# Performance work log

Hardware: AMD Instinct MI355X
Metric: run time of the kernel (lower is better)

The kernel has to match this reference:

```python
import jax, jax.numpy as jnp
import numpy as np

V, NJ, NCOMP, NBETA = 778, 16, 24, 10
F_CLOSED, N_ANCHOR = 1554, 32
B, NOBJ = 8, 16384
# MANO kinematic tree parents (wrist + 5 fingers x 3 joints)
PARENTS = np.array([-1, 0, 1, 2, 0, 4, 5, 0, 7, 8, 0, 10, 11, 0, 13, 14])


def setup_inputs() -> dict:
    key = jax.random.key(0)
    ks = jax.random.split(key, 12)
    hand_pose = jax.random.normal(ks[0], (B, 3 + 3 + NCOMP), jnp.float32) * 0.1
    obj_points = jax.random.normal(ks[1], (B, NOBJ, 3), jnp.float32) * 0.1
    hand_beta = jax.random.normal(ks[2], (B, NBETA), jnp.float32) * 0.5
    v_template = jax.random.normal(ks[3], (V, 3), jnp.float32) * 0.05
    shapedirs = jax.random.normal(ks[4], (V, 3, NBETA), jnp.float32) * 0.01
    posedirs = jax.random.normal(ks[5], (V, 3, (NJ - 1) * 9), jnp.float32) * 0.01
    J_regressor = jax.nn.softmax(jax.random.normal(ks[6], (NJ, V), jnp.float32), axis=-1)
    lbs_weights = jax.nn.softmax(jax.random.normal(ks[7], (V, NJ), jnp.float32) * 2.0, axis=-1)
    pca_comps = jax.random.normal(ks[8], (NCOMP, (NJ - 1) * 3), jnp.float32) * 0.1
    anchor_weights = jax.nn.softmax(jax.random.normal(ks[9], (N_ANCHOR, 3), jnp.float32), axis=-1)
    closed_faces = jax.random.randint(ks[10], (F_CLOSED, 3), 0, V, jnp.int32)
    anchor_face_idx = jax.random.randint(ks[11], (N_ANCHOR, 3), 0, V, jnp.int32)
    return dict(hand_pose=hand_pose, obj_points=obj_points, hand_beta=hand_beta,
                v_template=v_template, shapedirs=shapedirs, posedirs=posedirs,
                J_regressor=J_regressor, lbs_weights=lbs_weights, pca_comps=pca_comps,
                anchor_weights=anchor_weights, closed_faces=closed_faces,
                anchor_face_idx=anchor_face_idx)


def rodrigues(r):
    # r: [..., 3] axis-angle -> [..., 3, 3] rotation matrix
    theta = jnp.sqrt(jnp.sum(r * r, axis=-1, keepdims=True) + 1e-16)
    k = r / theta
    c = jnp.cos(theta)[..., None]
    s = jnp.sin(theta)[..., None]
    kx, ky, kz = k[..., 0], k[..., 1], k[..., 2]
    zero = jnp.zeros_like(kx)
    K = jnp.stack([zero, -kz, ky, kz, zero, -kx, -ky, kx, zero], axis=-1)
    K = K.reshape(r.shape[:-1] + (3, 3))
    I = jnp.eye(3, dtype=r.dtype)
    return c * I + s * K + (1.0 - c) * k[..., :, None] * k[..., None, :]


def mano_verts(hand_pose, hand_beta, v_template, shapedirs, posedirs,
               J_regressor, lbs_weights, pca_comps):
    b = hand_pose.shape[0]
    trans = hand_pose[:, :3]
    root = hand_pose[:, 3:6]
    hand45 = hand_pose[:, 6:] @ pca_comps  # PCA -> 45-dim pose (flat_hand_mean: no mean add)
    full = jnp.concatenate([root, hand45], axis=-1).reshape(b, NJ, 3)
    R = rodrigues(full)  # [B,16,3,3]
    v_shaped = v_template + jnp.einsum('vdk,bk->bvd', shapedirs, hand_beta)
    J = jnp.einsum('jv,bvd->bjd', J_regressor, v_shaped)  # [B,16,3]
    pose_feat = (R[:, 1:] - jnp.eye(3, dtype=R.dtype)).reshape(b, (NJ - 1) * 9)
    v_posed = v_shaped + jnp.einsum('vdp,bp->bvd', posedirs, pose_feat)

    def make44(Rj, tj):  # [B,3,3],[B,3] -> [B,4,4]
        T = jnp.zeros((b, 4, 4), R.dtype)
        return T.at[:, :3, :3].set(Rj).at[:, :3, 3].set(tj).at[:, 3, 3].set(1.0)

    Ts = [make44(R[:, 0], J[:, 0])]
    for j in range(1, NJ):  # fixed small kinematic chain
        p = int(PARENTS[j])
        Ts.append(jnp.einsum('bmn,bnk->bmk', Ts[p], make44(R[:, j], J[:, j] - J[:, p])))
    T = jnp.stack(Ts, axis=1)  # [B,16,4,4] global joint transforms
    corr = jnp.einsum('bjmn,bjn->bjm', T[..., :3, :3], J)
    A = T.at[..., :3, 3].add(-corr)  # relative-to-rest transforms
    Tw = jnp.einsum('vj,bjmn->bvmn', lbs_weights, A)  # per-vertex skinning transform
    verts = jnp.einsum('bvmn,bvn->bvm', Tw[..., :3, :3], v_posed) + Tw[..., :3, 3]
    return verts + trans[:, None, :]


def vertex_normals(verts, faces):  # verts [B,V,3], faces [F,3]
    def one(v):
        p0, p1, p2 = v[faces[:, 0]], v[faces[:, 1]], v[faces[:, 2]]
        fn = jnp.cross(p1 - p0, p2 - p0)
        vn = (jnp.zeros_like(v).at[faces[:, 0]].add(fn)
              .at[faces[:, 1]].add(fn).at[faces[:, 2]].add(fn))
        return vn / (jnp.linalg.norm(vn, axis=-1, keepdims=True) + 1e-8)
    return jax.vmap(one)(verts)


def reference(hand_pose, obj_points, hand_beta, v_template, shapedirs, posedirs,
              J_regressor, lbs_weights, pca_comps, anchor_weights,
              closed_faces, anchor_face_idx):
    verts = mano_verts(hand_pose, hand_beta, v_template, shapedirs, posedirs,
                       J_regressor, lbs_weights, pca_comps)  # [B,778,3]
    # get_NN: squared cdist obj->hand + argmin (the memory-bound bottleneck)
    d2 = (jnp.sum(obj_points * obj_points, -1, keepdims=True)
          + jnp.sum(verts * verts, -1)[:, None, :]
          - 2.0 * jnp.einsum('bnd,bvd->bnv', obj_points, verts))  # [B,NOBJ,778]
    nn_idx = jnp.argmin(d2, axis=-1)  # [B,NOBJ]
    nn_dist = jnp.take_along_axis(d2, nn_idx[..., None], axis=-1)[..., 0]
    # contact_map_of_m_to_n
    cmap = 1.0 - 2.0 * (jax.nn.sigmoid(100.0 * nn_dist) - 0.5)
    # inter_penetr_loss: interior obj points (behind nearest hand vertex normal)
    normals = vertex_normals(verts, closed_faces)
    nn_vert = jnp.take_along_axis(verts, nn_idx[..., None], axis=1)
    nn_norm = jnp.take_along_axis(normals, nn_idx[..., None], axis=1)
    interior = jnp.sum((nn_vert - obj_points) * nn_norm, axis=-1) > 0.0
    penetration = jnp.sum(jnp.where(interior, nn_dist, 0.0)) / hand_pose.shape[0]
    # AnchorLayer: barycentric anchor points on the hand surface
    contact_candidates = jnp.einsum('ak,bakd->bad', anchor_weights, verts[:, anchor_face_idx])
    return cmap, penetration, verts, contact_candidates
```

## Files before the change

kernel.cpp:

```cpp
#include <hip/hip_runtime.h>
#include <math.h>

#define NV 778
#define NJ 16
#define NCOMP 24
#define NBETA 10
#define FC 1554
#define NA 32
#define NB 8
#define NOBJ 16384
#define VD (NV*3)
#define NSLOT 13

__global__ __launch_bounds__(256) void k_blend(
    const float* __restrict__ hp, const float* __restrict__ pca,
    const float* __restrict__ beta, const float* __restrict__ vt,
    const float* __restrict__ sd, const float* __restrict__ pd,
    float* __restrict__ VS, float* __restrict__ VP, float* __restrict__ pen)
{
    int b = blockIdx.x >> 2, chunk = blockIdx.x & 3, t = threadIdx.x;
    __shared__ float h45[45];
    __shared__ float sR[NJ*9];
    __shared__ float PF[135];
    if (t < 45) {
        float acc = 0.0f;
        for (int k = 0; k < NCOMP; ++k) acc += hp[b*30 + 6 + k] * pca[k*45 + t];
        h45[t] = acc;
    }
    __syncthreads();
    if (t < NJ) {
        float rx, ry, rz;
        if (t == 0) { rx = hp[b*30+3]; ry = hp[b*30+4]; rz = hp[b*30+5]; }
        else        { rx = h45[(t-1)*3]; ry = h45[(t-1)*3+1]; rz = h45[(t-1)*3+2]; }
        float th = sqrtf(rx*rx + ry*ry + rz*rz + 1e-16f);
        float kx = rx/th, ky = ry/th, kz = rz/th;
        float c = cosf(th), s = sinf(th), o = 1.0f - c;
        sR[t*9+0] = c + o*kx*kx;      sR[t*9+1] = -s*kz + o*kx*ky;  sR[t*9+2] =  s*ky + o*kx*kz;
        sR[t*9+3] =  s*kz + o*ky*kx;  sR[t*9+4] = c + o*ky*ky;      sR[t*9+5] = -s*kx + o*ky*kz;
        sR[t*9+6] = -s*ky + o*kz*kx;  sR[t*9+7] =  s*kx + o*kz*ky;  sR[t*9+8] = c + o*kz*kz;
    }
    __syncthreads();
    if (t < 135) {
        int mn = t % 9;
        float d = (mn == 0 || mn == 4 || mn == 8) ? 1.0f : 0.0f;
        PF[t] = sR[9 + t] - d;
    }
    __syncthreads();
    int v = chunk * 195 + t;
    if (t < 195 && v < NV) {
        const float* bb = beta + b * NBETA;
        int i = b * NV + v;
        #pragma unroll
        for (int d = 0; d < 3; ++d) {
            int r = v*3 + d;
            float vs = vt[r];
            const float* s = sd + r * NBETA;
            #pragma unroll
            for (int k = 0; k < NBETA; ++k) vs += s[k] * bb[k];
            float vp = vs;
            const float* p = pd + r * 135;
            for (int k = 0; k < 135; ++k) vp += p[k] * PF[k];
            VS[i*3 + d] = vs;
            VP[i*3 + d] = vp;
        }
    }
    if (blockIdx.x == 0 && t == 0) *pen = 0.0f;
}

__global__ __launch_bounds__(256) void k_skel(
    const float* __restrict__ hp, const float* __restrict__ pca,
    const float* __restrict__ Jreg, const float* __restrict__ VS,
    const float* __restrict__ VP, const float* __restrict__ W,
    const int* __restrict__ faces, const float* __restrict__ aw,
    const int* __restrict__ afi,
    float* __restrict__ verts, float4* __restrict__ PK,
    float* __restrict__ NRM, float* __restrict__ contact)
{
    int b = blockIdx.x, t = threadIdx.x;
    int lane = t & 63, wid = t >> 6;
    __shared__ float h45[45];
    __shared__ float sR[NJ*9];
    __shared__ float sJ[NJ*3];
    __shared__ float sA[NJ*12];
    __shared__ float sv[VD];
    __shared__ float sn[VD];

    if (t < 45) {
        float acc = 0.0f;
        for (int k = 0; k < NCOMP; ++k) acc += hp[b*30 + 6 + k] * pca[k*45 + t];
        h45[t] = acc;
    }
    for (int i = t; i < VD; i += 256) sn[i] = 0.0f;
    __syncthreads();
    if (t < NJ) {
        float rx, ry, rz;
        if (t == 0) { rx = hp[b*30+3]; ry = hp[b*30+4]; rz = hp[b*30+5]; }
        else        { rx = h45[(t-1)*3]; ry = h45[(t-1)*3+1]; rz = h45[(t-1)*3+2]; }
        float th = sqrtf(rx*rx + ry*ry + rz*rz + 1e-16f);
        float kx = rx/th, ky = ry/th, kz = rz/th;
        float c = cosf(th), s = sinf(th), o = 1.0f - c;
        sR[t*9+0] = c + o*kx*kx;      sR[t*9+1] = -s*kz + o*kx*ky;  sR[t*9+2] =  s*ky + o*kx*kz;
        sR[t*9+3] =  s*kz + o*ky*kx;  sR[t*9+4] = c + o*ky*ky;      sR[t*9+5] = -s*kx + o*ky*kz;
        sR[t*9+6] = -s*ky + o*kz*kx;  sR[t*9+7] =  s*kx + o*kz*ky;  sR[t*9+8] = c + o*kz*kz;
    }

    float ac[12];
    #pragma unroll
    for (int q = 0; q < 12; ++q) ac[q] = 0.0f;
    for (int v = lane; v < NV; v += 64) {
        const float* p = VS + (b*NV + v)*3;
        float x = p[0], y = p[1], z = p[2];
        #pragma unroll
        for (int jj = 0; jj < 4; ++jj) {
            float w = Jreg[(4*wid + jj)*NV + v];
            ac[jj*3+0] += w*x; ac[jj*3+1] += w*y; ac[jj*3+2] += w*z;
        }
    }
    #pragma unroll
    for (int q = 0; q < 12; ++q)
        for (int off = 32; off; off >>= 1) ac[q] += __shfl_down(ac[q], off, 64);
    if (lane == 0) {
        #pragma unroll
        for (int q = 0; q < 12; ++q) sJ[(4*wid + q/3)*3 + (q%3)] = ac[q];
    }
    __syncthreads();

    if (t < 3) {
        const int par[NJ] = {-1,0,1,2,0,4,5,0,7,8,0,10,11,0,13,14};
        int m = t;
        float Tr[NJ][3], Tt[NJ];
        Tr[0][0] = sR[m*3+0]; Tr[0][1] = sR[m*3+1]; Tr[0][2] = sR[m*3+2];
        Tt[0] = sJ[m];
        #pragma unroll
        for (int j = 1; j < NJ; ++j) {
            int p = par[j];
            float t0 = sJ[j*3+0] - sJ[p*3+0];
            float t1 = sJ[j*3+1] - sJ[p*3+1];
            float t2 = sJ[j*3+2] - sJ[p*3+2];
            float a0 = Tr[p][0], a1 = Tr[p][1], a2 = Tr[p][2];
            #pragma unroll
            for (int n = 0; n < 3; ++n)
                Tr[j][n] = a0*sR[j*9+n] + a1*sR[j*9+3+n] + a2*sR[j*9+6+n];
            Tt[j] = a0*t0 + a1*t1 + a2*t2 + Tt[p];
        }
        #pragma unroll
        for (int j = 0; j < NJ; ++j) {
            float corr = Tr[j][0]*sJ[j*3] + Tr[j][1]*sJ[j*3+1] + Tr[j][2]*sJ[j*3+2];
            sA[j*12 + m*4 + 0] = Tr[j][0];
            sA[j*12 + m*4 + 1] = Tr[j][1];
            sA[j*12 + m*4 + 2] = Tr[j][2];
            sA[j*12 + m*4 + 3] = Tt[j] - corr;
        }
    }
    __syncthreads();

    float tx = hp[b*30+0], ty = hp[b*30+1], tz = hp[b*30+2];
    for (int v = t; v < NV; v += 256) {
        float acc[12];
        #pragma unroll
        for (int q = 0; q < 12; ++q) acc[q] = 0.0f;
        const float* w = W + v * NJ;
        for (int j = 0; j < NJ; ++j) {
            float wj = w[j];
            #pragma unroll
            for (int q = 0; q < 12; ++q) acc[q] += wj * sA[j*12 + q];
        }
        int i = b*NV + v;
        float px = VP[i*3], py = VP[i*3+1], pz = VP[i*3+2];
        float x = acc[0]*px + acc[1]*py + acc[2]*pz  + acc[3]  + tx;
        float y = acc[4]*px + acc[5]*py + acc[6]*pz  + acc[7]  + ty;
        float z = acc[8]*px + acc[9]*py + acc[10]*pz + acc[11] + tz;
        sv[v*3] = x; sv[v*3+1] = y; sv[v*3+2] = z;
        verts[i*3] = x; verts[i*3+1] = y; verts[i*3+2] = z;
        PK[i] = make_float4(x, y, z, 0.5f*(x*x + y*y + z*z));
    }
    __syncthreads();

    for (int f = t; f < FC; f += 256) {
        int i0 = faces[f*3], i1 = faces[f*3+1], i2 = faces[f*3+2];
        float ax = sv[i1*3+0]-sv[i0*3+0], ay = sv[i1*3+1]-sv[i0*3+1], az = sv[i1*3+2]-sv[i0*3+2];
        float bx = sv[i2*3+0]-sv[i0*3+0], by = sv[i2*3+1]-sv[i0*3+1], bz = sv[i2*3+2]-sv[i0*3+2];
        float cx = ay*bz - az*by, cy = az*bx - ax*bz, cz = ax*by - ay*bx;
        atomicAdd(&sn[i0*3+0], cx); atomicAdd(&sn[i0*3+1], cy); atomicAdd(&sn[i0*3+2], cz);
        atomicAdd(&sn[i1*3+0], cx); atomicAdd(&sn[i1*3+1], cy); atomicAdd(&sn[i1*3+2], cz);
        atomicAdd(&sn[i2*3+0], cx); atomicAdd(&sn[i2*3+1], cy); atomicAdd(&sn[i2*3+2], cz);
    }
    __syncthreads();

    for (int i = t; i < VD; i += 256) NRM[b*VD + i] = sn[i];
    if (t < NA*3) {
        int a = t / 3, d = t % 3;
        float acc = 0.0f;
        #pragma unroll
        for (int k = 0; k < 3; ++k)
            acc += aw[a*3 + k] * sv[afi[a*3 + k]*3 + d];
        contact[b*NA*3 + t] = acc;
    }
}

__global__ __launch_bounds__(256) void k_nn(const float* __restrict__ obj,
                                            const float4* __restrict__ PK,
                                            const float* __restrict__ NRM,
                                            float* __restrict__ cmap,
                                            float* __restrict__ pen)
{
    int b = blockIdx.x >> 6;
    int n = (blockIdx.x & 63) * 256 + threadIdx.x;
    int t = threadIdx.x, lane = t & 63;
    int base = b * NV;

    float4 q[NSLOT];
    #pragma unroll
    for (int j = 0; j < NSLOT; ++j) {
        int idx = j*64 + lane;
        q[j] = (idx < NV) ? PK[base + idx] : make_float4(0.f, 0.f, 0.f, 1e30f);
    }
    const float* o = obj + (b*NOBJ + n)*3;
    float ox = o[0], oy = o[1], oz = o[2];

    float myS = 0.0f;
    int myI = 0;
    for (int p = 0; p < 64; ++p) {
        float bx = __uint_as_float(__builtin_amdgcn_readlane(__float_as_uint(ox), p));
        float by = __uint_as_float(__builtin_amdgcn_readlane(__float_as_uint(oy), p));
        float bz = __uint_as_float(__builtin_amdgcn_readlane(__float_as_uint(oz), p));
        float sb = 1e30f; int jb = 0;
        #pragma unroll
        for (int j = 0; j < NSLOT; ++j) {
            float s = fmaf(-bx, q[j].x, q[j].w);
            s = fmaf(-by, q[j].y, s);
            s = fmaf(-bz, q[j].z, s);
            if (s < sb) { sb = s; jb = j; }
        }
        int ifull = jb*64 + lane;
        float smin = sb;
        #pragma unroll
        for (int m = 1; m < 64; m <<= 1)
            smin = fminf(smin, __shfl_xor(smin, m, 64));
        unsigned long long mk = __ballot(sb == smin);
        int w = __ffsll(mk) - 1;
        int widx = __builtin_amdgcn_readlane(ifull, w);
        if (lane == p) { myS = smin; myI = widx; }
    }

    float osq = ox*ox + oy*oy + oz*oz;
    float d2 = 2.0f * myS + osq;
    cmap[b*NOBJ + n] = 2.0f / (1.0f + expf(100.0f * d2));

    float4 qq = PK[base + myI];
    float nx = NRM[(base + myI)*3 + 0];
    float ny = NRM[(base + myI)*3 + 1];
    float nz = NRM[(base + myI)*3 + 2];
    float dotp = (qq.x - ox)*nx + (qq.y - oy)*ny + (qq.z - oz)*nz;
    float p = (dotp > 0.0f) ? d2 : 0.0f;
    for (int off = 32; off; off >>= 1) p += __shfl_down(p, off, 64);
    __shared__ float wsum[4];
    if (lane == 0) wsum[t >> 6] = p;
    __syncthreads();
    if (t == 0) atomicAdd(pen, (wsum[0] + wsum[1] + wsum[2] + wsum[3]) * (1.0f / NB));
}

extern "C" void kernel_launch(void* const* d_in, const int* in_sizes, int n_in,
                              void* d_out, int out_size, void* d_ws, size_t ws_size,
                              hipStream_t stream)
{
    const float* hp    = (const float*)d_in[0];
    const float* obj   = (const float*)d_in[1];
    const float* beta  = (const float*)d_in[2];
    const float* vt    = (const float*)d_in[3];
    const float* sd    = (const float*)d_in[4];
    const float* pd    = (const float*)d_in[5];
    const float* Jreg  = (const float*)d_in[6];
    const float* W     = (const float*)d_in[7];
    const float* pca   = (const float*)d_in[8];
    const float* aw    = (const float*)d_in[9];
    const int*   faces = (const int*)d_in[10];
    const int*   afi   = (const int*)d_in[11];

    float* out     = (float*)d_out;
    float* cmap    = out;
    float* pen     = out + NB*NOBJ;
    float* verts   = out + NB*NOBJ + 1;
    float* contact = out + NB*NOBJ + 1 + NB*NV*3;

    float* ws  = (float*)d_ws;
    float4* PK = (float4*)ws;
    float* VS  = ws + NB*NV*4;
    float* VP  = VS + NB*NV*3;
    float* NRM = VP + NB*NV*3;

    k_blend<<<NB*4, 256, 0, stream>>>(hp, pca, beta, vt, sd, pd, VS, VP, pen);
    k_skel <<<NB, 256, 0, stream>>>(hp, pca, Jreg, VS, VP, W, faces, aw, afi,
                                    verts, PK, NRM, contact);
    k_nn   <<<NB*64, 256, 0, stream>>>(obj, PK, NRM, cmap, pen);
}
```

Baseline: 166.3 us.

## Fuse blend-shape and skeleton kernels into one per-batch prep kernel

Merges k_blend and k_skel into a single k_prep kernel with one block per batch element. Shaped vertices stay in shared memory and the pose blend is computed inline, which removes the VS/VP global round trip and one kernel launch. It also packs PF and the skinning matrices as float4 in shared memory. The cost is parallelism: the posedirs matvec now runs on 8 blocks instead of 32, so each thread handles more vertices (778 per block of 256).

```diff
diff --git a/kernel.cpp b/kernel.cpp
--- a/kernel.cpp
+++ b/kernel.cpp
@@ -12,22 +12,36 @@
 #define VD (NV*3)
 #define NSLOT 13
 
-__global__ __launch_bounds__(256) void k_blend(
+__global__ __launch_bounds__(256) void k_prep(
     const float* __restrict__ hp, const float* __restrict__ pca,
     const float* __restrict__ beta, const float* __restrict__ vt,
     const float* __restrict__ sd, const float* __restrict__ pd,
-    float* __restrict__ VS, float* __restrict__ VP, float* __restrict__ pen)
+    const float* __restrict__ Jreg, const float* __restrict__ W,
+    const int* __restrict__ faces, const float* __restrict__ aw,
+    const int* __restrict__ afi,
+    float* __restrict__ verts, float4* __restrict__ PK,
+    float* __restrict__ NRM, float* __restrict__ contact,
+    float* __restrict__ pen)
 {
-    int b = blockIdx.x >> 2, chunk = blockIdx.x & 3, t = threadIdx.x;
-    __shared__ float h45[45];
-    __shared__ float sR[NJ*9];
-    __shared__ float PF[135];
+    int b = blockIdx.x, t = threadIdx.x;
+    int lane = t & 63, wid = t >> 6;
+    __shared__ float  h45[45];
+    __shared__ float  sR[NJ*9];
+    __shared__ float4 PF4[34];
+    __shared__ float  sJ[NJ*3];
+    __shared__ float4 sA4[NJ*3];
+    __shared__ float  svs[VD];
+    __shared__ float  sv[VD];
+    __shared__ float  sn[VD];
+
     if (t < 45) {
         float acc = 0.0f;
         for (int k = 0; k < NCOMP; ++k) acc += hp[b*30 + 6 + k] * pca[k*45 + t];
         h45[t] = acc;
     }
-    __syncthreads();
+    for (int i = t; i < VD; i += 256) sn[i] = 0.0f;
+    __syncthreads();
+
     if (t < NJ) {
         float rx, ry, rz;
         if (t == 0) { rx = hp[b*30+3]; ry = hp[b*30+4]; rz = hp[b*30+5]; }
@@ -39,89 +53,43 @@
         sR[t*9+3] =  s*kz + o*ky*kx;  sR[t*9+4] = c + o*ky*ky;      sR[t*9+5] = -s*kx + o*ky*kz;
         sR[t*9+6] = -s*ky + o*kz*kx;  sR[t*9+7] =  s*kx + o*kz*ky;  sR[t*9+8] = c + o*kz*kz;
     }
-    __syncthreads();
+    {
+        const float* bb = beta + b * NBETA;
+        for (int r = t; r < VD; r += 256) {
+            float vs = vt[r];
+            const float* s = sd + r * NBETA;
+            #pragma unroll
+            for (int k = 0; k < NBETA; ++k) vs += s[k] * bb[k];
+            svs[r] = vs;
+        }
+    }
+    __syncthreads();
+
     if (t < 135) {
         int mn = t % 9;
         float d = (mn == 0 || mn == 4 || mn == 8) ? 1.0f : 0.0f;
-        PF[t] = sR[9 + t] - d;
-    }
-    __syncthreads();
-    int v = chunk * 195 + t;
-    if (t < 195 && v < NV) {
-        const float* bb = beta + b * NBETA;
-        int i = b * NV + v;
-        #pragma unroll
-        for (int d = 0; d < 3; ++d) {
-            int r = v*3 + d;
-            float vs = vt[r];
-            const float* s = sd + r * NBETA;
-            #pragma unroll
-            for (int k = 0; k < NBETA; ++k) vs += s[k] * bb[k];
-            float vp = vs;
-            const float* p = pd + r * 135;
-            for (int k = 0; k < 135; ++k) vp += p[k] * PF[k];
-            VS[i*3 + d] = vs;
-            VP[i*3 + d] = vp;
-        }
-    }
-    if (blockIdx.x == 0 && t == 0) *pen = 0.0f;
-}
-
-__global__ __launch_bounds__(256) void k_skel(
-    const float* __restrict__ hp, const float* __restrict__ pca,
-    const float* __restrict__ Jreg, const float* __restrict__ VS,
-    const float* __restrict__ VP, const float* __restrict__ W,
-    const int* __restrict__ faces, const float* __restrict__ aw,
-    const int* __restrict__ afi,
-    float* __restrict__ verts, float4* __restrict__ PK,
-    float* __restrict__ NRM, float* __restrict__ contact)
-{
-    int b = blockIdx.x, t = threadIdx.x;
-    int lane = t & 63, wid = t >> 6;
-    __shared__ float h45[45];
-    __shared__ float sR[NJ*9];
-    __shared__ float sJ[NJ*3];
-    __shared__ float sA[NJ*12];
-    __shared__ float sv[VD];
-    __shared__ float sn[VD];
-
-    if (t < 45) {
-        float acc = 0.0f;
-        for (int k = 0; k < NCOMP; ++k) acc += hp[b*30 + 6 + k] * pca[k*45 + t];
-        h45[t] = acc;
-    }
-    for (int i = t; i < VD; i += 256) sn[i] = 0.0f;
-    __syncthreads();
-    if (t < NJ) {
-        float rx, ry, rz;
-        if (t == 0) { rx = hp[b*30+3]; ry = hp[b*30+4]; rz = hp[b*30+5]; }
-        else        { rx = h45[(t-1)*3]; ry = h45[(t-1)*3+1]; rz = h45[(t-1)*3+2]; }
-        float th = sqrtf(rx*rx + ry*ry + rz*rz + 1e-16f);
-        float kx = rx/th, ky = ry/th, kz = rz/th;
-        float c = cosf(th), s = sinf(th), o = 1.0f - c;
-        sR[t*9+0] = c + o*kx*kx;      sR[t*9+1] = -s*kz + o*kx*ky;  sR[t*9+2] =  s*ky + o*kx*kz;
-        sR[t*9+3] =  s*kz + o*ky*kx;  sR[t*9+4] = c + o*ky*ky;      sR[t*9+5] = -s*kx + o*ky*kz;
-        sR[t*9+6] = -s*ky + o*kz*kx;  sR[t*9+7] =  s*kx + o*kz*ky;  sR[t*9+8] = c + o*kz*kz;
-    }
-
-    float ac[12];
-    #pragma unroll
-    for (int q = 0; q < 12; ++q) ac[q] = 0.0f;
-    for (int v = lane; v < NV; v += 64) {
-        const float* p = VS + (b*NV + v)*3;
-        float x = p[0], y = p[1], z = p[2];
-        #pragma unroll
-        for (int jj = 0; jj < 4; ++jj) {
-            float w = Jreg[(4*wid + jj)*NV + v];
-            ac[jj*3+0] += w*x; ac[jj*3+1] += w*y; ac[jj*3+2] += w*z;
-        }
-    }
-    #pragma unroll
-    for (int q = 0; q < 12; ++q)
-        for (int off = 32; off; off >>= 1) ac[q] += __shfl_down(ac[q], off, 64);
-    if (lane == 0) {
-        #pragma unroll
-        for (int q = 0; q < 12; ++q) sJ[(4*wid + q/3)*3 + (q%3)] = ac[q];
+        ((float*)PF4)[t] = sR[9 + t] - d;
+    }
+    if (t == 135) ((float*)PF4)[135] = 0.0f;
+    {
+        float ac[12];
+        #pragma unroll
+        for (int q = 0; q < 12; ++q) ac[q] = 0.0f;
+        for (int v = lane; v < NV; v += 64) {
+            float x = svs[v*3], y = svs[v*3+1], z = svs[v*3+2];
+            #pragma unroll
+            for (int jj = 0; jj < 4; ++jj) {
+                float w = Jreg[(4*wid + jj)*NV + v];
+                ac[jj*3+0] += w*x; ac[jj*3+1] += w*y; ac[jj*3+2] += w*z;
+            }
+        }
+        #pragma unroll
+        for (int q = 0; q < 12; ++q)
+            for (int off = 32; off; off >>= 1) ac[q] += __shfl_down(ac[q], off, 64);
+        if (lane == 0) {
+            #pragma unroll
+            for (int q = 0; q < 12; ++q) sJ[(4*wid + q/3)*3 + (q%3)] = ac[q];
+        }
     }
     __syncthreads();
 
@@ -146,30 +114,49 @@
         #pragma unroll
         for (int j = 0; j < NJ; ++j) {
             float corr = Tr[j][0]*sJ[j*3] + Tr[j][1]*sJ[j*3+1] + Tr[j][2]*sJ[j*3+2];
-            sA[j*12 + m*4 + 0] = Tr[j][0];
-            sA[j*12 + m*4 + 1] = Tr[j][1];
-            sA[j*12 + m*4 + 2] = Tr[j][2];
-            sA[j*12 + m*4 + 3] = Tt[j] - corr;
+            sA4[j*3 + m] = make_float4(Tr[j][0], Tr[j][1], Tr[j][2], Tt[j] - corr);
         }
     }
     __syncthreads();
 
     float tx = hp[b*30+0], ty = hp[b*30+1], tz = hp[b*30+2];
     for (int v = t; v < NV; v += 256) {
-        float acc[12];
-        #pragma unroll
-        for (int q = 0; q < 12; ++q) acc[q] = 0.0f;
+        const float* p0 = pd + v * 405;
+        float a0 = 0.f, a1 = 0.f, a2 = 0.f;
+        #pragma unroll 4
+        for (int kb = 0; kb < 33; ++kb) {
+            float4 pf = PF4[kb];
+            int k = kb * 4;
+            a0 = fmaf(p0[k+0],     pf.x, a0); a0 = fmaf(p0[k+1],     pf.y, a0);
+            a0 = fmaf(p0[k+2],     pf.z, a0); a0 = fmaf(p0[k+3],     pf.w, a0);
+            a1 = fmaf(p0[135+k+0], pf.x, a1); a1 = fmaf(p0[135+k+1], pf.y, a1);
+            a1 = fmaf(p0[135+k+2], pf.z, a1); a1 = fmaf(p0[135+k+3], pf.w, a1);
+            a2 = fmaf(p0[270+k+0], pf.x, a2); a2 = fmaf(p0[270+k+1], pf.y, a2);
+            a2 = fmaf(p0[270+k+2], pf.z, a2); a2 = fmaf(p0[270+k+3], pf.w, a2);
+        }
+        #pragma unroll
+        for (int k = 132; k < 135; ++k) {
+            float pf = ((const float*)PF4)[k];
+            a0 = fmaf(p0[k], pf, a0);
+            a1 = fmaf(p0[135+k], pf, a1);
+            a2 = fmaf(p0[270+k], pf, a2);
+        }
+        float px = svs[v*3]   + a0;
+        float py = svs[v*3+1] + a1;
+        float pz = svs[v*3+2] + a2;
+        float4 r0 = make_float4(0,0,0,0), r1 = make_float4(0,0,0,0), r2 = make_float4(0,0,0,0);
         const float* w = W + v * NJ;
         for (int j = 0; j < NJ; ++j) {
             float wj = w[j];
-            #pragma unroll
-            for (int q = 0; q < 12; ++q) acc[q] += wj * sA[j*12 + q];
+            float4 A0 = sA4[j*3+0], A1 = sA4[j*3+1], A2 = sA4[j*3+2];
+            r0.x += wj*A0.x; r0.y += wj*A0.y; r0.z += wj*A0.z; r0.w += wj*A0.w;
+            r1.x += wj*A1.x; r1.y += wj*A1.y; r1.z += wj*A1.z; r1.w += wj*A1.w;
+            r2.x += wj*A2.x; r2.y += wj*A2.y; r2.z += wj*A2.z; r2.w += wj*A2.w;
         }
         int i = b*NV + v;
-        float px = VP[i*3], py = VP[i*3+1], pz = VP[i*3+2];
-        float x = acc[0]*px + acc[1]*py + acc[2]*pz  + acc[3]  + tx;
-        float y = acc[4]*px + acc[5]*py + acc[6]*pz  + acc[7]  + ty;
-        float z = acc[8]*px + acc[9]*py + acc[10]*pz + acc[11] + tz;
+        float x = r0.x*px + r0.y*py + r0.z*pz + r0.w + tx;
+        float y = r1.x*px + r1.y*py + r1.z*pz + r1.w + ty;
+        float z = r2.x*px + r2.y*py + r2.z*pz + r2.w + tz;
         sv[v*3] = x; sv[v*3+1] = y; sv[v*3+2] = z;
         verts[i*3] = x; verts[i*3+1] = y; verts[i*3+2] = z;
         PK[i] = make_float4(x, y, z, 0.5f*(x*x + y*y + z*z));
@@ -196,6 +183,7 @@
             acc += aw[a*3 + k] * sv[afi[a*3 + k]*3 + d];
         contact[b*NA*3 + t] = acc;
     }
+    if (b == 0 && t == 0) *pen = 0.0f;
 }
 
 __global__ __launch_bounds__(256) void k_nn(const float* __restrict__ obj,
@@ -285,12 +273,9 @@
 
     float* ws  = (float*)d_ws;
     float4* PK = (float4*)ws;
-    float* VS  = ws + NB*NV*4;
-    float* VP  = VS + NB*NV*3;
-    float* NRM = VP + NB*NV*3;
-
-    k_blend<<<NB*4, 256, 0, stream>>>(hp, pca, beta, vt, sd, pd, VS, VP, pen);
-    k_skel <<<NB, 256, 0, stream>>>(hp, pca, Jreg, VS, VP, W, faces, aw, afi,
-                                    verts, PK, NRM, contact);
-    k_nn   <<<NB*64, 256, 0, stream>>>(obj, PK, NRM, cmap, pen);
+    float* NRM = ws + NB*NV*4;
+
+    k_prep<<<NB, 256, 0, stream>>>(hp, pca, beta, vt, sd, pd, Jreg, W,
+                                   faces, aw, afi, verts, PK, NRM, contact, pen);
+    k_nn  <<<NB*64, 256, 0, stream>>>(obj, PK, NRM, cmap, pen);
 }
```

New measurement: 214.2 us. 28.8% more time.
